# Kernel optimization log

Hardware: AMD Instinct MI355X
Metric: run time of the kernel (lower is better)

Reference implementation:

```python
import jax, jax.numpy as jnp
import numpy as np

BS, NA, NE_, NL = 128, 3, 3, 3
NALL = NA - 1                 # n_allies
ENT = NA + NE_ + NL           # 9 entities
EM1 = ENT - 1                 # 8
HID = 64                      # hidden_dim
HEAD = 4
HIN = 9                       # hyper input dim
HYP = 64                      # hyper hidden dim
NRBF, RUB = 3, 10.0
EPS = 1e-7


def _lin_init(k, fan_in, fan_out):
    k1, k2 = jax.random.split(k)
    lim = 1.0 / np.sqrt(fan_in)
    w = jax.random.uniform(k1, (fan_in, fan_out), minval=-lim, maxval=lim, dtype=jnp.float32)
    b = jax.random.uniform(k2, (fan_out,), minval=-lim, maxval=lim, dtype=jnp.float32)
    return w, b


def setup_inputs():
    key = jax.random.key(0)
    ks = jax.random.split(key, 12)
    d = {}
    obs_dim = 4 + 2 * (NL + NALL + NE_) + 2 * (NALL + NE_)  # 30
    d["inputs"] = jax.random.normal(ks[0], (BS * NA, obs_dim), dtype=jnp.float32)
    d["hidden_state"] = jnp.zeros((1, HID), dtype=jnp.float32)
    d["actions"] = jax.random.normal(ks[1], (BS * NA, 2), dtype=jnp.float32)
    out_dim = (HIN + 1) * HID * HEAD  # 2560
    d["hA1_w"], d["hA1_b"] = _lin_init(ks[2], HIN, HYP)
    d["hA2_w"], d["hA2_b"] = _lin_init(ks[3], HYP, out_dim)
    d["hE1_w"], d["hE1_b"] = _lin_init(ks[4], HIN, HYP)
    d["hE2_w"], d["hE2_b"] = _lin_init(ks[5], HYP, out_dim)
    d["hL1_w"], d["hL1_b"] = _lin_init(ks[6], HIN, HYP)
    d["hL2_w"], d["hL2_b"] = _lin_init(ks[7], HYP, out_dim)
    d["merger_w"] = jnp.ones((1, HEAD, HID), dtype=jnp.float32)
    d["fc1_w"], d["fc1_b"] = _lin_init(ks[8], HID + 3, HID)
    d["fc2_w"], d["fc2_b"] = _lin_init(ks[9], HID, 1)
    return d


def _pair_out(feat, w1, b1, w2, b2):
    # hypernetwork: Linear(9,64) -> LeakyReLU -> Linear(64, (9+1)*64*4)
    h = jax.nn.leaky_relu(feat @ w1 + b1, negative_slope=0.01)
    out = h @ w2 + b2                               # (bs,NA,EM1,EM1,2560)
    nw = HIN * HID * HEAD
    w = out[..., :nw].reshape(feat.shape[:-1] + (HIN, HID * HEAD))
    b = out[..., nw:]
    y = jnp.einsum('...k,...kd->...d', feat, w) + b  # tiny 1x9 @ 9x256 per pair
    return y.reshape(feat.shape[:-1] + (HEAD, HID))


def _forward(inputs, actions, hA1_w, hA1_b, hA2_w, hA2_b, hE1_w, hE1_b, hE2_w, hE2_b,
             hL1_w, hL1_b, hL2_w, hL2_b, merger_w, fc1_w, fc1_b, fc2_w, fc2_b):
    bs = inputs.shape[0] // NA
    ob = inputs
    own = ob[:, :4].reshape(bs, NA, 4)
    i = 4
    lm_pos = ob[:, i:i + NL * 2].reshape(bs, NA, NL, 2); i += NL * 2
    ally_pos = ob[:, i:i + NALL * 2].reshape(bs, NA, NALL, 2); i += NALL * 2
    enemy_pos = ob[:, i:i + NE_ * 2].reshape(bs, NA, NE_, 2); i += NE_ * 2
    entity_pos = jnp.concatenate([ally_pos, enemy_pos, lm_pos], axis=-2)  # (bs,NA,EM1,2)
    ally_vel = ob[:, i:i + NALL * 2].reshape(bs, NA, NALL, 2); i += NALL * 2
    enemy_vel = ob[:, i:i + NE_ * 2].reshape(bs, NA, NE_, 2)
    lm_vel = jnp.zeros_like(lm_pos) - own[:, :, None, :2]
    entity_vel = jnp.concatenate([ally_vel, enemy_vel, lm_vel], axis=-2)  # (bs,NA,EM1,2)
    # rel_vel[b,a,j,i] = vel[i] - vel[j]
    rel_vel = entity_vel[:, :, None, :, :] - entity_vel[:, :, :, None, :]
    vel_norm = jnp.sqrt((entity_vel ** 2).sum(-1))
    sin_a = entity_vel[..., 1] / (vel_norm + EPS)
    cos_a = entity_vel[..., 0] / (vel_norm + EPS)
    act = actions.reshape(bs, NA, 2)
    act_norm = jnp.sqrt((act ** 2).sum(-1))        # (bs,NA)
    sin_b = act[..., 1] / (act_norm + EPS)
    cos_b = act[..., 0] / (act_norm + EPS)
    dist = jnp.sqrt((entity_pos ** 2).sum(-1))     # (bs,NA,EM1)
    sin_t = entity_pos[..., 1] / (dist + EPS)
    cos_t = entity_pos[..., 0] / (dist + EPS)
    # pair angles: A,C vary over last axis (i), B over second-to-last (j)
    sA, cA = sin_t[:, :, None, :], cos_t[:, :, None, :]
    sB, cB = sin_t[:, :, :, None], cos_t[:, :, :, None]
    sC, cC = sin_a[:, :, None, :], cos_a[:, :, None, :]
    angle_info = jnp.stack([sA * cB - cA * sB, cA * cB + sA * sB,
                            sC * cB - cC * sB, cC * cB + sC * sB], axis=-1)
    angle_info = jnp.broadcast_to(angle_info, (bs, NA, EM1, EM1, 4))
    sD, cD = sin_b[:, :, None], cos_b[:, :, None]
    act_angle = jnp.stack([sD * cos_t - cD * sin_t, cD * cos_t + sD * sin_t], axis=-1)  # (bs,NA,EM1,2)
    # gaussian RBF (schnet-style smearing, num_rbf=3, rbound_upper=10)
    offset = jnp.linspace(0.0, RUB, NRBF)
    coeff = -0.5 / (offset[1] - offset[0]) ** 2
    rbf = jnp.exp(coeff * (dist[..., None] - offset) ** 2)  # (bs,NA,EM1,NRBF)
    feat_dist = jnp.broadcast_to(rbf[:, :, None, :, :], (bs, NA, EM1, EM1, NRBF))
    feat = jnp.concatenate([feat_dist, angle_info, rel_vel], axis=-1)  # (bs,NA,EM1,EM1,9)
    ally_out = _pair_out(feat, hA1_w, hA1_b, hA2_w, hA2_b)
    enemy_out = _pair_out(feat, hE1_w, hE1_b, hE2_w, hE2_b)
    lm_out = _pair_out(feat, hL1_w, hL1_b, hL2_w, hL2_b)
    # type-based selection over the source-entity axis (dim 3), then sum-aggregate
    m = jnp.concatenate([ally_out[:, :, :, :NALL],
                         enemy_out[:, :, :, NALL:NALL + NE_],
                         lm_out[:, :, :, NALL + NE_:]], axis=3)
    m_sum = m.sum(axis=3)                               # (bs,NA,EM1,HEAD,HID)
    mw = jax.nn.softmax(merger_w, axis=1)               # (1,HEAD,HID)
    m_jki = (mw * m_sum).sum(axis=-2)                   # (bs,NA,EM1,HID)
    an = jnp.broadcast_to(act_norm[:, :, None], (bs, NA, EM1))[..., None]
    final = jnp.concatenate([m_jki, an, act_angle], axis=-1)  # (bs,NA,EM1,HID+3)
    x = jax.nn.relu(final)
    x = jax.nn.relu(x @ fc1_w + fc1_b)
    q = (x @ fc2_w + fc2_b).mean(axis=-2).reshape(-1, 1)  # (bs*NA,1)
    return q, x


def reference(inputs, hidden_state, actions, hA1_w, hA1_b, hA2_w, hA2_b,
              hE1_w, hE1_b, hE2_w, hE2_b, hL1_w, hL1_b, hL2_w, hL2_b,
              merger_w, fc1_w, fc1_b, fc2_w, fc2_b):
    q, x = _forward(inputs, actions, hA1_w, hA1_b, hA2_w, hA2_b,
                    hE1_w, hE1_b, hE2_w, hE2_b, hL1_w, hL1_b, hL2_w, hL2_b,
                    merger_w, fc1_w, fc1_b, fc2_w, fc2_b)
    return q, x
```

## Files before the change

### kernel.cpp

```cpp
#include <hip/hip_runtime.h>
#include <math.h>

#define EPS 1e-7f
#define NETS 3
#define HROWP 384
#define HG    (HROWP/4)
#define GPW   (HG/4)
#define JSTRIDE (NETS*HROWP)
#define W2R_F4_TOT (2*NETS*HG*64)
#define ZPART_OFF 589824

__global__ __launch_bounds__(256) void prep_w2r(
    const float* __restrict__ W2A, const float* __restrict__ b2A,
    const float* __restrict__ W2E, const float* __restrict__ b2E,
    const float* __restrict__ W2L, const float* __restrict__ b2L,
    const float* __restrict__ merger, float* __restrict__ W2r)
{
    int idx = blockIdx.x * 256 + threadIdx.x;
    if (idx >= W2R_F4_TOT) return;
    int half = idx / (NETS*HG*64);
    int rem  = idx - half * (NETS*HG*64);
    int net  = rem / (HG*64);
    rem     -= net * (HG*64);
    int g4   = rem >> 6;
    int hid  = rem & 63;

    float m0 = merger[hid], m1 = merger[64+hid], m2 = merger[128+hid], m3 = merger[192+hid];
    float mx = fmaxf(fmaxf(m0, m1), fmaxf(m2, m3));
    float e0 = expf(m0-mx), e1 = expf(m1-mx), e2 = expf(m2-mx), e3 = expf(m3-mx);
    float inv = 1.0f / (e0+e1+e2+e3);
    float w0 = e0*inv, w1 = e1*inv, w2 = e2*inv, w3 = e3*inv;

    const float* W2 = (net==0) ? W2A : ((net==1) ? W2E : W2L);
    const float* b2 = (net==0) ? b2A : ((net==1) ? b2E : b2L);

    float4 v;
    float* vp = &v.x;
    #pragma unroll
    for (int r = 0; r < 4; ++r) {
        int row = g4*4 + r;
        float val = 0.0f;
        if (row < 325) {
            const float* src;
            int kk;
            if (row < 320) { kk = half*5 + (row >> 6); int h = row & 63; src = W2 + h*2560; }
            else           { kk = half*5 + (row - 320);                  src = b2; }
            int col = (kk < 9) ? kk*256 : 2304;
            val = w0*src[col+hid] + w1*src[col+64+hid] + w2*src[col+128+hid] + w3*src[col+192+hid];
        }
        vp[r] = val;
    }
    ((float4*)W2r)[idx] = v;
}

__global__ __launch_bounds__(256, 3) void half_kernel(
    const float* __restrict__ inputs, const float* __restrict__ actions,
    const float* __restrict__ W1A, const float* __restrict__ b1A,
    const float* __restrict__ W1E, const float* __restrict__ b1E,
    const float* __restrict__ W1L, const float* __restrict__ b1L,
    const float* __restrict__ W2r, float* __restrict__ Zpart)
{
    __shared__ __align__(16) float sU[8 * JSTRIDE];

    const int tid   = threadIdx.x;
    const int agent = blockIdx.x >> 1;
    const int half  = blockIdx.x & 1;
    const int lane  = tid & 63;
    const int w     = tid >> 6;
    const int q     = lane >> 4, hh = lane & 15;

    float w1r[3][9], b1r[3];
    {
        const float* Ws[3] = {W1A, W1E, W1L};
        const float* bs[3] = {b1A, b1E, b1L};
        #pragma unroll
        for (int net = 0; net < 3; ++net) {
            #pragma unroll
            for (int kk = 0; kk < 9; ++kk) w1r[net][kk] = Ws[net][kk*64 + lane];
            b1r[net] = bs[net][lane];
        }
    }

    const float4* Wbase = (const float4*)W2r + (size_t)half * (NETS*HG*64);
    const int base = w * GPW;
    float4 wk0, wk1, wk2, wk3;
    {
        int g = base + q;
        const float4* wb = Wbase + g*64 + hh;
        wk0 = wb[0]; wk1 = wb[16]; wk2 = wb[32]; wk3 = wb[48];
    }

    float ob = 0.0f;
    if (lane < 30)      ob = inputs[agent*30 + lane];
    else if (lane < 32) ob = actions[agent*2 + (lane - 30)];

    int e = lane & 7;
    int ppos, vpos; bool lm = false;
    if (e < 2)      { ppos = 10+2*e;     vpos = 20+2*e; }
    else if (e < 5) { ppos = 14+2*(e-2); vpos = 24+2*(e-2); }
    else            { ppos = 4+2*(e-5);  vpos = 0; lm = true; }
    float px = __shfl(ob, ppos), py = __shfl(ob, ppos+1);
    float vx = __shfl(ob, vpos), vy = __shfl(ob, vpos+1);
    if (lm) { vx = -vx; vy = -vy; }
    float d  = sqrtf(px*px + py*py);
    float st = py / (d + EPS), ct = px / (d + EPS);
    float vn = sqrtf(vx*vx + vy*vy);
    float sa = vy / (vn + EPS), ca = vx / (vn + EPS);
    float rb0 = expf(-0.02f * d * d);
    float d5  = d - 5.0f,  rb1 = expf(-0.02f * d5 * d5);
    float d10 = d - 10.0f, rb2 = expf(-0.02f * d10 * d10);

    int jj = lane >> 3;
    float st_j = __shfl(st, jj), ct_j = __shfl(ct, jj);
    float vx_j = __shfl(vx, jj), vy_j = __shfl(vy, jj);
    float f0 = rb0, f1 = rb1, f2 = rb2;
    float f3 = st*ct_j - ct*st_j;
    float f4 = ct*ct_j + st*st_j;
    float f5 = sa*ct_j - ca*st_j;
    float f6 = ca*ct_j + sa*st_j;
    float f7 = vx - vx_j;
    float f8 = vy - vy_j;

    #pragma unroll
    for (int t = 0; t < 2; ++t) {
        int j = 2*w + t;
        #pragma unroll
        for (int net = 0; net < NETS; ++net) {
            int ks = (net==0) ? 0 : ((net==1) ? 2 : 5);
            int kn = (net==0) ? 2 : 3;
            float v0=0.f,v1=0.f,v2=0.f,v3=0.f,v4=0.f;
            float gs0=0.f,gs1=0.f,gs2=0.f,gs3=0.f,gs4=0.f;
            for (int qq = 0; qq < kn; ++qq) {
                int p = j*8 + ks + qq;
                float s0=__shfl(f0,p), s1=__shfl(f1,p), s2=__shfl(f2,p);
                float s3=__shfl(f3,p), s4=__shfl(f4,p), s5=__shfl(f5,p);
                float s6=__shfl(f6,p), s7=__shfl(f7,p), s8=__shfl(f8,p);
                float acc = b1r[net];
                acc = fmaf(s0, w1r[net][0], acc);
                acc = fmaf(s1, w1r[net][1], acc);
                acc = fmaf(s2, w1r[net][2], acc);
                acc = fmaf(s3, w1r[net][3], acc);
                acc = fmaf(s4, w1r[net][4], acc);
                acc = fmaf(s5, w1r[net][5], acc);
                acc = fmaf(s6, w1r[net][6], acc);
                acc = fmaf(s7, w1r[net][7], acc);
                acc = fmaf(s8, w1r[net][8], acc);
                float H = (acc > 0.0f) ? acc : 0.01f*acc;
                float g0 = half ? s5 : s0;
                float g1 = half ? s6 : s1;
                float g2 = half ? s7 : s2;
                float g3 = half ? s8 : s3;
                float g4 = half ? 1.0f : s4;
                v0 = fmaf(H, g0, v0);  gs0 += g0;
                v1 = fmaf(H, g1, v1);  gs1 += g1;
                v2 = fmaf(H, g2, v2);  gs2 += g2;
                v3 = fmaf(H, g3, v3);  gs3 += g3;
                v4 = fmaf(H, g4, v4);  gs4 += g4;
            }
            float* dst = sU + (j*NETS + net)*HROWP + lane;
            dst[0]   = v0;
            dst[64]  = v1;
            dst[128] = v2;
            dst[192] = v3;
            dst[256] = v4;
            float bv = 0.0f;
            bv = (lane==0) ? gs0 : bv;
            bv = (lane==1) ? gs1 : bv;
            bv = (lane==2) ? gs2 : bv;
            bv = (lane==3) ? gs3 : bv;
            bv = (lane==4) ? gs4 : bv;
            dst[320] = bv;
        }
    }
    __syncthreads();

    float acc[8][4];
    #pragma unroll
    for (int j = 0; j < 8; ++j)
        #pragma unroll
        for (int k = 0; k < 4; ++k) acc[j][k] = 0.0f;

    for (int it = 0; it < 18; ++it) {
        int net = it / 6, u = it - net*6;
        int g = base + u*4 + q;
        float4 nk0, nk1, nk2, nk3;
        if (it < 17) {
            int nit = it + 1;
            int nnet = nit / 6, nu_ = nit - nnet*6;
            int ng = base + nu_*4 + q;
            const float4* wb = Wbase + (nnet*HG + ng)*64 + hh;
            nk0 = wb[0]; nk1 = wb[16]; nk2 = wb[32]; nk3 = wb[48];
        }
        const float* Ub = sU + net*HROWP + g*4;
        #pragma unroll
        for (int j = 0; j < 8; ++j) {
            float4 uu = *(const float4*)(Ub + j*JSTRIDE);
            acc[j][0] = fmaf(uu.x,wk0.x, fmaf(uu.y,wk0.y, fmaf(uu.z,wk0.z, fmaf(uu.w,wk0.w, acc[j][0]))));
            acc[j][1] = fmaf(uu.x,wk1.x, fmaf(uu.y,wk1.y, fmaf(uu.z,wk1.z, fmaf(uu.w,wk1.w, acc[j][1]))));
            acc[j][2] = fmaf(uu.x,wk2.x, fmaf(uu.y,wk2.y, fmaf(uu.z,wk2.z, fmaf(uu.w,wk2.w, acc[j][2]))));
            acc[j][3] = fmaf(uu.x,wk3.x, fmaf(uu.y,wk3.y, fmaf(uu.z,wk3.z, fmaf(uu.w,wk3.w, acc[j][3]))));
        }
        wk0 = nk0; wk1 = nk1; wk2 = nk2; wk3 = nk3;
    }

    float* zb = Zpart + (((size_t)agent*2 + half)*4 + w) * 512;
    #pragma unroll
    for (int j = 0; j < 8; ++j) {
        float v0 = acc[j][0]; v0 += __shfl_xor(v0,16); v0 += __shfl_xor(v0,32);
        float v1 = acc[j][1]; v1 += __shfl_xor(v1,16); v1 += __shfl_xor(v1,32);
        float v2 = acc[j][2]; v2 += __shfl_xor(v2,16); v2 += __shfl_xor(v2,32);
        float v3 = acc[j][3]; v3 += __shfl_xor(v3,16); v3 += __shfl_xor(v3,32);
        float out = (q==0) ? v0 : ((q==1) ? v1 : ((q==2) ? v2 : v3));
        zb[j*64 + lane] = out;
    }
}

__global__ __launch_bounds__(256) void epilogue_kernel(
    const float* __restrict__ inputs, const float* __restrict__ actions,
    const float* __restrict__ Zpart,
    const float* __restrict__ fc1w, const float* __restrict__ fc1b,
    const float* __restrict__ fc2w, const float* __restrict__ fc2b,
    float* __restrict__ out_q, float* __restrict__ out_x)
{
    __shared__ float sOb[32];
    __shared__ float sSt[8], sCt[8];
    __shared__ float sAct[3];
    __shared__ float sZ[8][64];
    __shared__ float sRed[4];

    const int tid   = threadIdx.x;
    const int agent = blockIdx.x;

    if (tid < 30) sOb[tid] = inputs[agent*30 + tid];
    if (tid == 30) sOb[30] = actions[agent*2 + 0];
    if (tid == 31) sOb[31] = actions[agent*2 + 1];
    __syncthreads();

    if (tid < 8) {
        int e = tid;
        float px, py;
        if (e < 2)      {           px = sOb[10+2*e]; py = sOb[11+2*e]; }
        else if (e < 5) { int t=e-2; px = sOb[14+2*t]; py = sOb[15+2*t]; }
        else            { int t=e-5; px = sOb[4+2*t];  py = sOb[5+2*t]; }
        float d = sqrtf(px*px + py*py);
        sSt[e] = py / (d + EPS);
        sCt[e] = px / (d + EPS);
    }
    if (tid == 8) {
        float ax = sOb[30], ay = sOb[31];
        float an = sqrtf(ax*ax + ay*ay);
        sAct[0] = an;
        sAct[1] = ay / (an + EPS);
        sAct[2] = ax / (an + EPS);
    }
    const float* Zp = Zpart + (size_t)agent*4096;
    for (int o = tid; o < 512; o += 256) {
        float z = 0.0f;
        #pragma unroll
        for (int c = 0; c < 8; ++c) z += Zp[c*512 + o];
        ((float*)sZ)[o] = (z > 0.0f) ? z : 0.0f;
    }
    __syncthreads();

    float an  = sAct[0], sb = sAct[1], cb = sAct[2];
    float anr = (an > 0.0f) ? an : 0.0f;
    float myq = 0.0f;
    #pragma unroll
    for (int i = 0; i < 2; ++i) {
        int o = i*256 + tid;
        int j = o >> 6, c = o & 63;
        float acc = fc1b[c];
        #pragma unroll 8
        for (int d = 0; d < 64; ++d)
            acc = fmaf(sZ[j][d], fc1w[d*64 + c], acc);
        float aa0 = sb*sCt[j] - cb*sSt[j];
        float aa1 = cb*sCt[j] + sb*sSt[j];
        aa0 = (aa0 > 0.0f) ? aa0 : 0.0f;
        aa1 = (aa1 > 0.0f) ? aa1 : 0.0f;
        acc = fmaf(anr, fc1w[64*64 + c], acc);
        acc = fmaf(aa0, fc1w[65*64 + c], acc);
        acc = fmaf(aa1, fc1w[66*64 + c], acc);
        float x1 = (acc > 0.0f) ? acc : 0.0f;
        out_x[(agent*8 + j)*64 + c] = x1;
        myq = fmaf(x1, fc2w[c], myq);
    }
    for (int off = 32; off; off >>= 1) myq += __shfl_down(myq, off);
    int lane = tid & 63, w = tid >> 6;
    if (lane == 0) sRed[w] = myq;
    __syncthreads();
    if (tid == 0) out_q[agent] = (sRed[0] + sRed[1] + sRed[2] + sRed[3]) * 0.125f + fc2b[0];
}

extern "C" void kernel_launch(void* const* d_in, const int* in_sizes, int n_in,
                              void* d_out, int out_size, void* d_ws, size_t ws_size,
                              hipStream_t stream) {
    const float* inputs  = (const float*)d_in[0];
    const float* actions = (const float*)d_in[2];
    const float* hA1_w = (const float*)d_in[3];  const float* hA1_b = (const float*)d_in[4];
    const float* hA2_w = (const float*)d_in[5];  const float* hA2_b = (const float*)d_in[6];
    const float* hE1_w = (const float*)d_in[7];  const float* hE1_b = (const float*)d_in[8];
    const float* hE2_w = (const float*)d_in[9];  const float* hE2_b = (const float*)d_in[10];
    const float* hL1_w = (const float*)d_in[11]; const float* hL1_b = (const float*)d_in[12];
    const float* hL2_w = (const float*)d_in[13]; const float* hL2_b = (const float*)d_in[14];
    const float* merger = (const float*)d_in[15];
    const float* fc1w = (const float*)d_in[16];  const float* fc1b = (const float*)d_in[17];
    const float* fc2w = (const float*)d_in[18];  const float* fc2b = (const float*)d_in[19];

    float* W2r   = (float*)d_ws;
    float* Zpart = (float*)((char*)d_ws + ZPART_OFF);
    float* q     = (float*)d_out;
    float* x     = q + 384;

    prep_w2r<<<(W2R_F4_TOT + 255)/256, 256, 0, stream>>>(
        hA2_w, hA2_b, hE2_w, hE2_b, hL2_w, hL2_b, merger, W2r);
    half_kernel<<<768, 256, 0, stream>>>(
        inputs, actions, hA1_w, hA1_b, hE1_w, hE1_b, hL1_w, hL1_b, W2r, Zpart);
    epilogue_kernel<<<384, 256, 0, stream>>>(
        inputs, actions, Zpart, fc1w, fc1b, fc2w, fc2b, q, x);
}
```

Measured before the change: 121.6 us.

## Merge half and epilogue kernels into one per-agent kernel

Replaces the two-blocks-per-agent split (each block covering half of the hyper-output rows) with one block per agent that processes all 650 rows, and folds the fc1/fc2 epilogue into the same kernel. The cross-wave partial sums are reduced in shared memory, so the Zpart round trip through global memory and one kernel launch go away. In exchange, grid parallelism is halved (384 blocks instead of 768), shared memory per block nearly doubles, and occupancy drops to 2 blocks per CU.

```diff
diff --git a/kernel.cpp b/kernel.cpp
--- a/kernel.cpp
+++ b/kernel.cpp
@@ -3,12 +3,12 @@
 
 #define EPS 1e-7f
 #define NETS 3
-#define HROWP 384
-#define HG    (HROWP/4)
-#define GPW   (HG/4)
-#define JSTRIDE (NETS*HROWP)
-#define W2R_F4_TOT (2*NETS*HG*64)
-#define ZPART_OFF 589824
+#define ROWP 656
+#define NROW_TOT (NETS*ROWP)
+#define G4 164
+#define GPW 41
+#define PERNET4 (G4*64)
+#define W2R_F4_TOT (NETS*PERNET4)
 
 __global__ __launch_bounds__(256) void prep_w2r(
     const float* __restrict__ W2A, const float* __restrict__ b2A,
@@ -18,12 +18,10 @@
 {
     int idx = blockIdx.x * 256 + threadIdx.x;
     if (idx >= W2R_F4_TOT) return;
-    int half = idx / (NETS*HG*64);
-    int rem  = idx - half * (NETS*HG*64);
-    int net  = rem / (HG*64);
-    rem     -= net * (HG*64);
-    int g4   = rem >> 6;
-    int hid  = rem & 63;
+    int net = idx / PERNET4;
+    int rem = idx - net * PERNET4;
+    int g4  = rem >> 6;
+    int hid = rem & 63;
 
     float m0 = merger[hid], m1 = merger[64+hid], m2 = merger[128+hid], m3 = merger[192+hid];
     float mx = fmaxf(fmaxf(m0, m1), fmaxf(m2, m3));
@@ -40,11 +38,11 @@
     for (int r = 0; r < 4; ++r) {
         int row = g4*4 + r;
         float val = 0.0f;
-        if (row < 325) {
+        if (row < 650) {
             const float* src;
             int kk;
-            if (row < 320) { kk = half*5 + (row >> 6); int h = row & 63; src = W2 + h*2560; }
-            else           { kk = half*5 + (row - 320);                  src = b2; }
+            if (row < 640) { kk = row >> 6; int h = row & 63; src = W2 + h*2560; }
+            else           { kk = row - 640;                  src = b2; }
             int col = (kk < 9) ? kk*256 : 2304;
             val = w0*src[col+hid] + w1*src[col+64+hid] + w2*src[col+128+hid] + w3*src[col+192+hid];
         }
@@ -53,18 +51,22 @@
     ((float4*)W2r)[idx] = v;
 }
 
-__global__ __launch_bounds__(256, 3) void half_kernel(
+__global__ __launch_bounds__(256, 2) void agent_kernel(
     const float* __restrict__ inputs, const float* __restrict__ actions,
     const float* __restrict__ W1A, const float* __restrict__ b1A,
     const float* __restrict__ W1E, const float* __restrict__ b1E,
     const float* __restrict__ W1L, const float* __restrict__ b1L,
-    const float* __restrict__ W2r, float* __restrict__ Zpart)
+    const float* __restrict__ W2r,
+    const float* __restrict__ fc1w, const float* __restrict__ fc1b,
+    const float* __restrict__ fc2w, const float* __restrict__ fc2b,
+    float* __restrict__ out_q, float* __restrict__ out_x)
 {
-    __shared__ __align__(16) float sU[8 * JSTRIDE];
+    __shared__ __align__(16) float sU[8 * NROW_TOT];
+    __shared__ float sSt[8], sCt[8], sAct[3];
+    __shared__ float sRed[4];
 
     const int tid   = threadIdx.x;
-    const int agent = blockIdx.x >> 1;
-    const int half  = blockIdx.x & 1;
+    const int agent = blockIdx.x;
     const int lane  = tid & 63;
     const int w     = tid >> 6;
     const int q     = lane >> 4, hh = lane & 15;
@@ -81,12 +83,12 @@
         }
     }
 
-    const float4* Wbase = (const float4*)W2r + (size_t)half * (NETS*HG*64);
+    const float4* Wp = (const float4*)W2r;
     const int base = w * GPW;
     float4 wk0, wk1, wk2, wk3;
     {
         int g = base + q;
-        const float4* wb = Wbase + g*64 + hh;
+        const float4* wb = Wp + g*64 + hh;
         wk0 = wb[0]; wk1 = wb[16]; wk2 = wb[32]; wk3 = wb[48];
     }
 
@@ -95,13 +97,13 @@
     else if (lane < 32) ob = actions[agent*2 + (lane - 30)];
 
     int e = lane & 7;
-    int ppos, vpos; bool lm = false;
+    int ppos, vpos; bool lmk = false;
     if (e < 2)      { ppos = 10+2*e;     vpos = 20+2*e; }
     else if (e < 5) { ppos = 14+2*(e-2); vpos = 24+2*(e-2); }
-    else            { ppos = 4+2*(e-5);  vpos = 0; lm = true; }
+    else            { ppos = 4+2*(e-5);  vpos = 0; lmk = true; }
     float px = __shfl(ob, ppos), py = __shfl(ob, ppos+1);
     float vx = __shfl(ob, vpos), vy = __shfl(ob, vpos+1);
-    if (lm) { vx = -vx; vy = -vy; }
+    if (lmk) { vx = -vx; vy = -vy; }
     float d  = sqrtf(px*px + py*py);
     float st = py / (d + EPS), ct = px / (d + EPS);
     float vn = sqrtf(vx*vx + vy*vy);
@@ -109,6 +111,13 @@
     float rb0 = expf(-0.02f * d * d);
     float d5  = d - 5.0f,  rb1 = expf(-0.02f * d5 * d5);
     float d10 = d - 10.0f, rb2 = expf(-0.02f * d10 * d10);
+
+    if (w == 0 && lane < 8) { sSt[lane] = st; sCt[lane] = ct; }
+    float ax = __shfl(ob, 30), ay = __shfl(ob, 31);
+    if (tid == 0) {
+        float an = sqrtf(ax*ax + ay*ay);
+        sAct[0] = an; sAct[1] = ay/(an+EPS); sAct[2] = ax/(an+EPS);
+    }
 
     int jj = lane >> 3;
     float st_j = __shfl(st, jj), ct_j = __shfl(ct, jj);
@@ -128,8 +137,8 @@
         for (int net = 0; net < NETS; ++net) {
             int ks = (net==0) ? 0 : ((net==1) ? 2 : 5);
             int kn = (net==0) ? 2 : 3;
-            float v0=0.f,v1=0.f,v2=0.f,v3=0.f,v4=0.f;
-            float gs0=0.f,gs1=0.f,gs2=0.f,gs3=0.f,gs4=0.f;
+            float v0=0.f,v1=0.f,v2=0.f,v3=0.f,v4=0.f,v5=0.f,v6=0.f,v7=0.f,v8=0.f,v9=0.f;
+            float g0s=0.f,g1s=0.f,g2s=0.f,g3s=0.f,g4s=0.f,g5s=0.f,g6s=0.f,g7s=0.f,g8s=0.f;
             for (int qq = 0; qq < kn; ++qq) {
                 int p = j*8 + ks + qq;
                 float s0=__shfl(f0,p), s1=__shfl(f1,p), s2=__shfl(f2,p);
@@ -146,30 +155,42 @@
                 acc = fmaf(s7, w1r[net][7], acc);
                 acc = fmaf(s8, w1r[net][8], acc);
                 float H = (acc > 0.0f) ? acc : 0.01f*acc;
-                float g0 = half ? s5 : s0;
-                float g1 = half ? s6 : s1;
-                float g2 = half ? s7 : s2;
-                float g3 = half ? s8 : s3;
-                float g4 = half ? 1.0f : s4;
-                v0 = fmaf(H, g0, v0);  gs0 += g0;
-                v1 = fmaf(H, g1, v1);  gs1 += g1;
-                v2 = fmaf(H, g2, v2);  gs2 += g2;
-                v3 = fmaf(H, g3, v3);  gs3 += g3;
-                v4 = fmaf(H, g4, v4);  gs4 += g4;
+                v0 = fmaf(H, s0, v0);  g0s += s0;
+                v1 = fmaf(H, s1, v1);  g1s += s1;
+                v2 = fmaf(H, s2, v2);  g2s += s2;
+                v3 = fmaf(H, s3, v3);  g3s += s3;
+                v4 = fmaf(H, s4, v4);  g4s += s4;
+                v5 = fmaf(H, s5, v5);  g5s += s5;
+                v6 = fmaf(H, s6, v6);  g6s += s6;
+                v7 = fmaf(H, s7, v7);  g7s += s7;
+                v8 = fmaf(H, s8, v8);  g8s += s8;
+                v9 += H;
             }
-            float* dst = sU + (j*NETS + net)*HROWP + lane;
-            dst[0]   = v0;
-            dst[64]  = v1;
-            dst[128] = v2;
-            dst[192] = v3;
-            dst[256] = v4;
-            float bv = 0.0f;
-            bv = (lane==0) ? gs0 : bv;
-            bv = (lane==1) ? gs1 : bv;
-            bv = (lane==2) ? gs2 : bv;
-            bv = (lane==3) ? gs3 : bv;
-            bv = (lane==4) ? gs4 : bv;
-            dst[320] = bv;
+            float* dst = sU + (j*NETS + net)*ROWP + lane;
+            dst[0]     = v0;
+            dst[64]    = v1;
+            dst[128]   = v2;
+            dst[192]   = v3;
+            dst[256]   = v4;
+            dst[320]   = v5;
+            dst[384]   = v6;
+            dst[448]   = v7;
+            dst[512]   = v8;
+            dst[576]   = v9;
+            if (lane < 16) {
+                float bv = 0.0f;
+                bv = (lane==0) ? g0s : bv;
+                bv = (lane==1) ? g1s : bv;
+                bv = (lane==2) ? g2s : bv;
+                bv = (lane==3) ? g3s : bv;
+                bv = (lane==4) ? g4s : bv;
+                bv = (lane==5) ? g5s : bv;
+                bv = (lane==6) ? g6s : bv;
+                bv = (lane==7) ? g7s : bv;
+                bv = (lane==8) ? g8s : bv;
+                bv = (lane==9) ? (float)kn : bv;
+                sU[(j*NETS + net)*ROWP + 640 + lane] = bv;
+            }
         }
     }
     __syncthreads();
@@ -180,115 +201,88 @@
         #pragma unroll
         for (int k = 0; k < 4; ++k) acc[j][k] = 0.0f;
 
-    for (int it = 0; it < 18; ++it) {
-        int net = it / 6, u = it - net*6;
-        int g = base + u*4 + q;
+    for (int it = 0; it < 33; ++it) {
+        int net = it / 11, u = it - net*11;
+        int g = base + ((u == 10) ? 40 : u*4 + q);
         float4 nk0, nk1, nk2, nk3;
-        if (it < 17) {
+        if (it < 32) {
             int nit = it + 1;
-            int nnet = nit / 6, nu_ = nit - nnet*6;
-            int ng = base + nu_*4 + q;
-            const float4* wb = Wbase + (nnet*HG + ng)*64 + hh;
+            int nnet = nit / 11, nu = nit - nnet*11;
+            int ng = base + ((nu == 10) ? 40 : nu*4 + q);
+            const float4* wb = Wp + (nnet*G4 + ng)*64 + hh;
             nk0 = wb[0]; nk1 = wb[16]; nk2 = wb[32]; nk3 = wb[48];
         }
-        const float* Ub = sU + net*HROWP + g*4;
-        #pragma unroll
-        for (int j = 0; j < 8; ++j) {
-            float4 uu = *(const float4*)(Ub + j*JSTRIDE);
-            acc[j][0] = fmaf(uu.x,wk0.x, fmaf(uu.y,wk0.y, fmaf(uu.z,wk0.z, fmaf(uu.w,wk0.w, acc[j][0]))));
-            acc[j][1] = fmaf(uu.x,wk1.x, fmaf(uu.y,wk1.y, fmaf(uu.z,wk1.z, fmaf(uu.w,wk1.w, acc[j][1]))));
-            acc[j][2] = fmaf(uu.x,wk2.x, fmaf(uu.y,wk2.y, fmaf(uu.z,wk2.z, fmaf(uu.w,wk2.w, acc[j][2]))));
-            acc[j][3] = fmaf(uu.x,wk3.x, fmaf(uu.y,wk3.y, fmaf(uu.z,wk3.z, fmaf(uu.w,wk3.w, acc[j][3]))));
+        if (u != 10 || q == 0) {
+            const float* Ub = sU + net*ROWP + g*4;
+            #pragma unroll
+            for (int j = 0; j < 8; ++j) {
+                float4 uu = *(const float4*)(Ub + j*NROW_TOT);
+                acc[j][0] = fmaf(uu.x,wk0.x, fmaf(uu.y,wk0.y, fmaf(uu.z,wk0.z, fmaf(uu.w,wk0.w, acc[j][0]))));
+                acc[j][1] = fmaf(uu.x,wk1.x, fmaf(uu.y,wk1.y, fmaf(uu.z,wk1.z, fmaf(uu.w,wk1.w, acc[j][1]))));
+                acc[j][2] = fmaf(uu.x,wk2.x, fmaf(uu.y,wk2.y, fmaf(uu.z,wk2.z, fmaf(uu.w,wk2.w, acc[j][2]))));
+                acc[j][3] = fmaf(uu.x,wk3.x, fmaf(uu.y,wk3.y, fmaf(uu.z,wk3.z, fmaf(uu.w,wk3.w, acc[j][3]))));
+            }
         }
         wk0 = nk0; wk1 = nk1; wk2 = nk2; wk3 = nk3;
     }
 
-    float* zb = Zpart + (((size_t)agent*2 + half)*4 + w) * 512;
+    float vr[8][4];
     #pragma unroll
-    for (int j = 0; j < 8; ++j) {
-        float v0 = acc[j][0]; v0 += __shfl_xor(v0,16); v0 += __shfl_xor(v0,32);
-        float v1 = acc[j][1]; v1 += __shfl_xor(v1,16); v1 += __shfl_xor(v1,32);
-        float v2 = acc[j][2]; v2 += __shfl_xor(v2,16); v2 += __shfl_xor(v2,32);
-        float v3 = acc[j][3]; v3 += __shfl_xor(v3,16); v3 += __shfl_xor(v3,32);
-        float out = (q==0) ? v0 : ((q==1) ? v1 : ((q==2) ? v2 : v3));
-        zb[j*64 + lane] = out;
-    }
-}
-
-__global__ __launch_bounds__(256) void epilogue_kernel(
-    const float* __restrict__ inputs, const float* __restrict__ actions,
-    const float* __restrict__ Zpart,
-    const float* __restrict__ fc1w, const float* __restrict__ fc1b,
-    const float* __restrict__ fc2w, const float* __restrict__ fc2b,
-    float* __restrict__ out_q, float* __restrict__ out_x)
-{
-    __shared__ float sOb[32];
-    __shared__ float sSt[8], sCt[8];
-    __shared__ float sAct[3];
-    __shared__ float sZ[8][64];
-    __shared__ float sRed[4];
-
-    const int tid   = threadIdx.x;
-    const int agent = blockIdx.x;
-
-    if (tid < 30) sOb[tid] = inputs[agent*30 + tid];
-    if (tid == 30) sOb[30] = actions[agent*2 + 0];
-    if (tid == 31) sOb[31] = actions[agent*2 + 1];
+    for (int j = 0; j < 8; ++j)
+        #pragma unroll
+        for (int k = 0; k < 4; ++k) {
+            float v = acc[j][k];
+            v += __shfl_xor(v, 16);
+            v += __shfl_xor(v, 32);
+            vr[j][k] = v;
+        }
     __syncthreads();
-
-    if (tid < 8) {
-        int e = tid;
-        float px, py;
-        if (e < 2)      {           px = sOb[10+2*e]; py = sOb[11+2*e]; }
-        else if (e < 5) { int t=e-2; px = sOb[14+2*t]; py = sOb[15+2*t]; }
-        else            { int t=e-5; px = sOb[4+2*t];  py = sOb[5+2*t]; }
-        float d = sqrtf(px*px + py*py);
-        sSt[e] = py / (d + EPS);
-        sCt[e] = px / (d + EPS);
-    }
-    if (tid == 8) {
-        float ax = sOb[30], ay = sOb[31];
-        float an = sqrtf(ax*ax + ay*ay);
-        sAct[0] = an;
-        sAct[1] = ay / (an + EPS);
-        sAct[2] = ax / (an + EPS);
-    }
-    const float* Zp = Zpart + (size_t)agent*4096;
+    {
+        float* sZp = sU;
+        if (q == 0) {
+            #pragma unroll
+            for (int j = 0; j < 8; ++j)
+                #pragma unroll
+                for (int k = 0; k < 4; ++k)
+                    sZp[(w*8 + j)*64 + k*16 + hh] = vr[j][k];
+        }
+    }
+    __syncthreads();
+    float* sZ = sU + 2048;
     for (int o = tid; o < 512; o += 256) {
-        float z = 0.0f;
-        #pragma unroll
-        for (int c = 0; c < 8; ++c) z += Zp[c*512 + o];
-        ((float*)sZ)[o] = (z > 0.0f) ? z : 0.0f;
+        float z = sU[o] + sU[512+o] + sU[1024+o] + sU[1536+o];
+        sZ[o] = (z > 0.0f) ? z : 0.0f;
     }
     __syncthreads();
 
-    float an  = sAct[0], sb = sAct[1], cb = sAct[2];
-    float anr = (an > 0.0f) ? an : 0.0f;
-    float myq = 0.0f;
-    #pragma unroll
-    for (int i = 0; i < 2; ++i) {
-        int o = i*256 + tid;
-        int j = o >> 6, c = o & 63;
-        float acc = fc1b[c];
-        #pragma unroll 8
-        for (int d = 0; d < 64; ++d)
-            acc = fmaf(sZ[j][d], fc1w[d*64 + c], acc);
-        float aa0 = sb*sCt[j] - cb*sSt[j];
-        float aa1 = cb*sCt[j] + sb*sSt[j];
-        aa0 = (aa0 > 0.0f) ? aa0 : 0.0f;
-        aa1 = (aa1 > 0.0f) ? aa1 : 0.0f;
-        acc = fmaf(anr, fc1w[64*64 + c], acc);
-        acc = fmaf(aa0, fc1w[65*64 + c], acc);
-        acc = fmaf(aa1, fc1w[66*64 + c], acc);
-        float x1 = (acc > 0.0f) ? acc : 0.0f;
-        out_x[(agent*8 + j)*64 + c] = x1;
-        myq = fmaf(x1, fc2w[c], myq);
-    }
-    for (int off = 32; off; off >>= 1) myq += __shfl_down(myq, off);
-    int lane = tid & 63, w = tid >> 6;
-    if (lane == 0) sRed[w] = myq;
-    __syncthreads();
-    if (tid == 0) out_q[agent] = (sRed[0] + sRed[1] + sRed[2] + sRed[3]) * 0.125f + fc2b[0];
+    {
+        float an  = sAct[0], sb = sAct[1], cb = sAct[2];
+        float anr = (an > 0.0f) ? an : 0.0f;
+        float myq = 0.0f;
+        #pragma unroll
+        for (int i = 0; i < 2; ++i) {
+            int o = i*256 + tid;
+            int j = o >> 6, c = o & 63;
+            float a1 = fc1b[c];
+            #pragma unroll 8
+            for (int dd = 0; dd < 64; ++dd)
+                a1 = fmaf(sZ[j*64 + dd], fc1w[dd*64 + c], a1);
+            float aa0 = sb*sCt[j] - cb*sSt[j];
+            float aa1 = cb*sCt[j] + sb*sSt[j];
+            aa0 = (aa0 > 0.0f) ? aa0 : 0.0f;
+            aa1 = (aa1 > 0.0f) ? aa1 : 0.0f;
+            a1 = fmaf(anr, fc1w[64*64 + c], a1);
+            a1 = fmaf(aa0, fc1w[65*64 + c], a1);
+            a1 = fmaf(aa1, fc1w[66*64 + c], a1);
+            float x1 = (a1 > 0.0f) ? a1 : 0.0f;
+            out_x[(agent*8 + j)*64 + c] = x1;
+            myq = fmaf(x1, fc2w[c], myq);
+        }
+        for (int off = 32; off; off >>= 1) myq += __shfl_down(myq, off);
+        if (lane == 0) sRed[w] = myq;
+        __syncthreads();
+        if (tid == 0) out_q[agent] = (sRed[0] + sRed[1] + sRed[2] + sRed[3]) * 0.125f + fc2b[0];
+    }
 }
 
 extern "C" void kernel_launch(void* const* d_in, const int* in_sizes, int n_in,
@@ -306,15 +300,13 @@
     const float* fc1w = (const float*)d_in[16];  const float* fc1b = (const float*)d_in[17];
     const float* fc2w = (const float*)d_in[18];  const float* fc2b = (const float*)d_in[19];
 
-    float* W2r   = (float*)d_ws;
-    float* Zpart = (float*)((char*)d_ws + ZPART_OFF);
-    float* q     = (float*)d_out;
-    float* x     = q + 384;
+    float* W2r = (float*)d_ws;
+    float* q   = (float*)d_out;
+    float* x   = q + 384;
 
     prep_w2r<<<(W2R_F4_TOT + 255)/256, 256, 0, stream>>>(
         hA2_w, hA2_b, hE2_w, hE2_b, hL2_w, hL2_b, merger, W2r);
-    half_kernel<<<768, 256, 0, stream>>>(
-        inputs, actions, hA1_w, hA1_b, hE1_w, hE1_b, hL1_w, hL1_b, W2r, Zpart);
-    epilogue_kernel<<<384, 256, 0, stream>>>(
-        inputs, actions, Zpart, fc1w, fc1b, fc2w, fc2b, q, x);
+    agent_kernel<<<384, 256, 0, stream>>>(
+        inputs, actions, hA1_w, hA1_b, hE1_w, hE1_b, hL1_w, hL1_b,
+        W2r, fc1w, fc1b, fc2w, fc2b, q, x);
 }
```

Result: slower. 124.3 us (+2.2%).
